# Performance work log

Measured on AMD Instinct MI355X. Metric: run time of the kernel, lower is better.

Reference implementation:

```python
import jax, jax.numpy as jnp
import numpy as np

B, S, D, H = 1, 4096, 1024, 16
HD = D // H  # 64


def setup_inputs() -> dict:
    key = jax.random.key(0)
    k1, k2, k3, k4, k5 = jax.random.split(key, 5)
    hidden_states = jax.random.normal(k1, (B, S, D), dtype=jnp.float32)
    # rotary frequencies: freqs_cis[s, j] = exp(i * s * theta^(-2j/HD)), stored as (cos, sin)
    inv_freq = 1.0 / (10000.0 ** (jnp.arange(0, HD, 2, dtype=jnp.float32) / HD))  # [HD/2]
    angles = jnp.arange(S, dtype=jnp.float32)[:, None] * inv_freq[None, :]        # [S, HD/2]
    freqs_cis = jnp.stack([jnp.cos(angles), jnp.sin(angles)], axis=-1)            # [S, HD/2, 2]
    attention_mask = jnp.ones((B, S), dtype=jnp.float32)
    scale = 1.0 / np.sqrt(D)
    wq = jax.random.normal(k2, (D, D), dtype=jnp.float32) * scale
    wk = jax.random.normal(k3, (D, D), dtype=jnp.float32) * scale
    wv = jax.random.normal(k4, (D, D), dtype=jnp.float32) * scale
    wo = jax.random.normal(k5, (D, D), dtype=jnp.float32) * scale
    return {"hidden_states": hidden_states, "freqs_cis": freqs_cis,
            "attention_mask": attention_mask, "wq": wq, "wk": wk, "wv": wv, "wo": wo}


def _apply_rope(x, freqs_cis):
    # x: [B, S, H, HD]; freqs_cis: [S, HD/2, 2] (cos, sin)
    b, s, h, hd = x.shape
    xr = x.reshape(b, s, h, hd // 2, 2)
    a, bb = xr[..., 0], xr[..., 1]
    cos = freqs_cis[None, :s, None, :, 0]
    sin = freqs_cis[None, :s, None, :, 1]
    out_r = a * cos - bb * sin
    out_i = a * sin + bb * cos
    return jnp.stack([out_r, out_i], axis=-1).reshape(b, s, h, hd)


def reference(hidden_states, freqs_cis, attention_mask, wq, wk, wv, wo):
    b, s, d = hidden_states.shape
    scaling = HD ** -0.5
    q = (hidden_states @ wq).reshape(b, s, H, HD)
    k = (hidden_states @ wk).reshape(b, s, H, HD)
    v = (hidden_states @ wv).reshape(b, s, H, HD)
    q = _apply_rope(q, freqs_cis)
    k = _apply_rope(k, freqs_cis)
    # [B, H, S, S] scores, exactly as the torch module materializes them
    scores = jnp.einsum('bqhd,bkhd->bhqk', q, k) * scaling
    mask_add = (1.0 - attention_mask)[:, None, None, :] * -10000.0  # [B,1,1,S]
    scores = scores + mask_add
    attn = jax.nn.softmax(scores.astype(jnp.float32), axis=-1).astype(q.dtype)
    out = jnp.einsum('bhqk,bkhd->bqhd', attn, v).reshape(b, s, d)
    return out @ wo
```

## Files before the change

### kernel.cpp

```cpp
#include <hip/hip_runtime.h>
#include <stdint.h>

#define S_LEN 4096
#define DMODEL 1024
#define NH 16
#define HDIM 64
#define KSPLIT 2
#define KCHUNK (S_LEN / KSPLIT)
#define LOG2E 1.44269504088896340736f

typedef __attribute__((ext_vector_type(8))) __bf16 bf16x8;
typedef __attribute__((ext_vector_type(4))) __bf16 bf16x4;
typedef __attribute__((ext_vector_type(2))) __bf16 bf16x2;
typedef __attribute__((ext_vector_type(4))) float f32x4;
typedef __attribute__((ext_vector_type(16))) float f32x16;
typedef __attribute__((ext_vector_type(4))) unsigned int uint32x4;

__global__ __launch_bounds__(256) void convert_f32_bf16(const float* __restrict__ src,
                                                        __bf16* __restrict__ dst,
                                                        const float* __restrict__ mask,
                                                        float* __restrict__ maskadd) {
  int idx = blockIdx.x * 256 + threadIdx.x;
  f32x4 v = ((const f32x4*)src)[idx];
  bf16x4 o;
#pragma unroll
  for (int i = 0; i < 4; ++i) o[i] = (__bf16)v[i];
  ((bf16x4*)dst)[idx] = o;
  if (idx < S_LEN) maskadd[idx] = (1.0f - mask[idx]) * (-10000.0f * LOG2E);
}

template <typename T>
__global__ __launch_bounds__(256) void transpose_tiles(const T* __restrict__ src,
                                                       __bf16* __restrict__ dst,
                                                       int R, int C) {
  src += (size_t)blockIdx.z * R * C;
  dst += (size_t)blockIdx.z * R * C;
  __shared__ __bf16 tile[64][65];
  const int r0 = blockIdx.y * 64, c0 = blockIdx.x * 64;
  const int t = threadIdx.x;
  const int col = t & 63, rsub = t >> 6;
#pragma unroll
  for (int i = 0; i < 16; ++i) {
    int r = rsub + i * 4;
    tile[r][col] = (__bf16)src[(size_t)(r0 + r) * C + (c0 + col)];
  }
  __syncthreads();
#pragma unroll
  for (int i = 0; i < 16; ++i) {
    int r = rsub + i * 4;
    dst[(size_t)(c0 + r) * R + (r0 + col)] = tile[col][r];
  }
}

template <int EPI>
__global__ __launch_bounds__(256) void gemm_bt(const __bf16* __restrict__ A,
                                               const __bf16* __restrict__ BT,
                                               __bf16* __restrict__ Cq,
                                               __bf16* __restrict__ Ck,
                                               __bf16* __restrict__ Cv,
                                               float* __restrict__ Cout,
                                               int Kdim, int Ndim) {
  __shared__ __align__(16) __bf16 At[128][40];
  __shared__ __align__(16) __bf16 Bt[128][40];
  const int t = threadIdx.x;
  const int wave = t >> 6, lane = t & 63;
  const int wr = wave >> 1, wc = wave & 1;
  const int lrow = lane & 15, lk = lane >> 4;
  const int bm = blockIdx.x, bn = blockIdx.y;

  f32x4 acc[4][4];
#pragma unroll
  for (int i = 0; i < 4; ++i)
#pragma unroll
    for (int j = 0; j < 4; ++j) acc[i][j] = f32x4{0.f, 0.f, 0.f, 0.f};

  const int arow0 = bm * 128, brow0 = bn * 128;
  for (int k0 = 0; k0 < Kdim; k0 += 32) {
    __syncthreads();
#pragma unroll
    for (int u = 0; u < 2; ++u) {
      int idx = t + u * 256;
      int row = idx >> 2, col = (idx & 3) * 8;
      *(bf16x8*)&At[row][col] =
          *(const bf16x8*)&A[(size_t)(arow0 + row) * Kdim + (k0 + col)];
      *(bf16x8*)&Bt[row][col] =
          *(const bf16x8*)&BT[(size_t)(brow0 + row) * Kdim + (k0 + col)];
    }
    __syncthreads();
    bf16x8 af[4], bfr[4];
#pragma unroll
    for (int mi = 0; mi < 4; ++mi)
      af[mi] = *(const bf16x8*)&At[wr * 64 + mi * 16 + lrow][lk * 8];
#pragma unroll
    for (int ni = 0; ni < 4; ++ni)
      bfr[ni] = *(const bf16x8*)&Bt[wc * 64 + ni * 16 + lrow][lk * 8];
#pragma unroll
    for (int mi = 0; mi < 4; ++mi)
#pragma unroll
      for (int ni = 0; ni < 4; ++ni)
        acc[mi][ni] =
            __builtin_amdgcn_mfma_f32_16x16x32_bf16(af[mi], bfr[ni], acc[mi][ni], 0, 0, 0);
  }

  const int rb = bm * 128 + wr * 64 + lk * 4;
  const int cb = bn * 128 + wc * 64 + lrow;
#pragma unroll
  for (int mi = 0; mi < 4; ++mi)
#pragma unroll
    for (int ni = 0; ni < 4; ++ni) {
      int c = cb + ni * 16;
#pragma unroll
      for (int r = 0; r < 4; ++r) {
        int row = rb + mi * 16 + r;
        float v = acc[mi][ni][r];
        if (EPI == 0) {
          Cout[(size_t)row * Ndim + c] = v;
        } else {
          int type = c >> 10, d = c & 1023;
          int hh = d >> 6, hd = d & 63;
          __bf16* dp = (type == 0) ? Cq : (type == 1) ? Ck : Cv;
          dp[((size_t)hh * S_LEN + row) * HDIM + hd] = (__bf16)v;
        }
      }
    }
}

__global__ __launch_bounds__(256) void rope_kernel(__bf16* __restrict__ Q,
                                                   __bf16* __restrict__ Kb,
                                                   const float* __restrict__ freqs) {
  size_t idx = (size_t)blockIdx.x * 256 + threadIdx.x;
  int i = idx & 31;
  size_t rest = idx >> 5;
  int s = rest & 4095;
  int h = (int)(rest >> 12);
  float c = freqs[(s * 32 + i) * 2 + 0];
  float sn = freqs[(s * 32 + i) * 2 + 1];
  size_t base = ((size_t)h * S_LEN + s) * HDIM + 2 * i;
  float qa = (float)Q[base], qb = (float)Q[base + 1];
  Q[base] = (__bf16)(qa * c - qb * sn);
  Q[base + 1] = (__bf16)(qa * sn + qb * c);
  float ka = (float)Kb[base], kb2 = (float)Kb[base + 1];
  Kb[base] = (__bf16)(ka * c - kb2 * sn);
  Kb[base + 1] = (__bf16)(ka * sn + kb2 * c);
}

__global__ __launch_bounds__(256, 4) void attn_split(const __bf16* __restrict__ Q,
                                                     const __bf16* __restrict__ Kmat,
                                                     const __bf16* __restrict__ Vt,
                                                     const float* __restrict__ maskadd,
                                                     float* __restrict__ Opart,
                                                     float* __restrict__ Lpart) {
  __shared__ __align__(16) __bf16 Kl[2][64][64];
  __shared__ __align__(16) __bf16 Vl[2][64][64];

  const int t = threadIdx.x;
  const int id = blockIdx.x;
  const int swz = (id & 7) * 128 + (id >> 3);
  const int h = swz >> 6;
  const int rem = swz & 63;
  const int qb = rem >> 1;
  const int split = rem & 1;
  const int k0 = split * KCHUNK;
  const int wave = t >> 6, lane = t & 63;
  const int lq = lane & 31, hi = lane >> 5;
  const int sw = lq & 7;

  const __bf16* Kh = Kmat + (size_t)h * S_LEN * HDIM;
  const __bf16* Vh = Vt + (size_t)h * HDIM * S_LEN;

  const int sr = t >> 2;
  const int sc0 = (t & 3) * 2;
  const int scs0 = (sc0 ^ (sr & 7)) * 8;
  const int scs1 = ((sc0 + 1) ^ (sr & 7)) * 8;
  const __bf16* Kgb = Kh + (size_t)sr * HDIM + sc0 * 8;
  const __bf16* Vgb = Vh + (size_t)sr * S_LEN + sc0 * 8;

  uint32x4 kreg0, kreg1, vreg0, vreg1;
  kreg0 = *(const uint32x4*)(Kgb + (size_t)k0 * HDIM);
  kreg1 = *(const uint32x4*)(Kgb + (size_t)k0 * HDIM + 8);
  vreg0 = *(const uint32x4*)(Vgb + k0);
  vreg1 = *(const uint32x4*)(Vgb + k0 + 8);
  *(uint32x4*)&Kl[0][sr][scs0] = kreg0;
  *(uint32x4*)&Kl[0][sr][scs1] = kreg1;
  *(uint32x4*)&Vl[0][sr][scs0] = vreg0;
  *(uint32x4*)&Vl[0][sr][scs1] = vreg1;

  const __bf16* Qh = Q + ((size_t)h * S_LEN + qb * 128 + wave * 32 + lq) * HDIM;
  bf16x8 qf[4];
#pragma unroll
  for (int ds = 0; ds < 4; ++ds) qf[ds] = *(const bf16x8*)(Qh + ds * 16 + hi * 8);

  __syncthreads();

  const float SCL = 0.125f * LOG2E;
  float l = 0.f;
  f32x16 o0, o1;
#pragma unroll
  for (int r = 0; r < 16; ++r) { o0[r] = 0.f; o1[r] = 0.f; }

  for (int it = 0; it < KCHUNK / 64; ++it) {
    const int cur = it & 1;
    const int kb = k0 + it * 64;

    if (it < KCHUNK / 64 - 1) {
      kreg0 = *(const uint32x4*)(Kgb + (size_t)(kb + 64) * HDIM);
      kreg1 = *(const uint32x4*)(Kgb + (size_t)(kb + 64) * HDIM + 8);
      vreg0 = *(const uint32x4*)(Vgb + (kb + 64));
      vreg1 = *(const uint32x4*)(Vgb + (kb + 64) + 8);
    }

    f32x16 p0, p1;
#pragma unroll
    for (int r = 0; r < 16; ++r) { p0[r] = 0.f; p1[r] = 0.f; }
    __builtin_amdgcn_s_setprio(1);
#pragma unroll
    for (int ds = 0; ds < 4; ++ds) {
      int sg = ((ds << 1) | hi) ^ sw;
      bf16x8 kf0 = *(const bf16x8*)&Kl[cur][lq][sg * 8];
      p0 = __builtin_amdgcn_mfma_f32_32x32x16_bf16(kf0, qf[ds], p0, 0, 0, 0);
    }
#pragma unroll
    for (int ds = 0; ds < 4; ++ds) {
      int sg = ((ds << 1) | hi) ^ sw;
      bf16x8 kf1 = *(const bf16x8*)&Kl[cur][lq + 32][sg * 8];
      p1 = __builtin_amdgcn_mfma_f32_32x32x16_bf16(kf1, qf[ds], p1, 0, 0, 0);
    }
    __builtin_amdgcn_s_setprio(0);

#pragma unroll
    for (int tq = 0; tq < 4; ++tq) {
      f32x4 ma0 = *(const f32x4*)&maskadd[kb + tq * 8 + hi * 4];
      f32x4 ma1 = *(const f32x4*)&maskadd[kb + 32 + tq * 8 + hi * 4];
#pragma unroll
      for (int c = 0; c < 4; ++c) {
        p0[tq * 4 + c] = exp2f(fmaf(p0[tq * 4 + c], SCL, ma0[c]));
        p1[tq * 4 + c] = exp2f(fmaf(p1[tq * 4 + c], SCL, ma1[c]));
      }
    }
    {
      float a0 = (p0[0] + p0[1]) + (p0[2] + p0[3]);
      float a1 = (p0[4] + p0[5]) + (p0[6] + p0[7]);
      float a2 = (p0[8] + p0[9]) + (p0[10] + p0[11]);
      float a3 = (p0[12] + p0[13]) + (p0[14] + p0[15]);
      float b0 = (p1[0] + p1[1]) + (p1[2] + p1[3]);
      float b1 = (p1[4] + p1[5]) + (p1[6] + p1[7]);
      float b2 = (p1[8] + p1[9]) + (p1[10] + p1[11]);
      float b3 = (p1[12] + p1[13]) + (p1[14] + p1[15]);
      float ps = ((a0 + a1) + (a2 + a3)) + ((b0 + b1) + (b2 + b3));
      ps += __shfl_xor(ps, 32);
      l += ps;
    }

    unsigned int tt0[8], tt1[8];
#pragma unroll
    for (int tp = 0; tp < 8; ++tp) {
      bf16x2 w0, w1;
      w0[0] = (__bf16)p0[2 * tp]; w0[1] = (__bf16)p0[2 * tp + 1];
      w1[0] = (__bf16)p1[2 * tp]; w1[1] = (__bf16)p1[2 * tp + 1];
      tt0[tp] = __builtin_bit_cast(unsigned int, w0);
      tt1[tp] = __builtin_bit_cast(unsigned int, w1);
    }

#pragma unroll
    for (int ks = 0; ks < 4; ++ks) {
      unsigned int b0, b1, b2, b3;
      if (ks == 0)      { b0 = tt0[0]; b1 = tt0[1]; b2 = tt0[2]; b3 = tt0[3]; }
      else if (ks == 1) { b0 = tt0[4]; b1 = tt0[5]; b2 = tt0[6]; b3 = tt0[7]; }
      else if (ks == 2) { b0 = tt1[0]; b1 = tt1[1]; b2 = tt1[2]; b3 = tt1[3]; }
      else              { b0 = tt1[4]; b1 = tt1[5]; b2 = tt1[6]; b3 = tt1[7]; }
      unsigned int send0 = hi ? b0 : b2;
      unsigned int send1 = hi ? b1 : b3;
      unsigned int r0 = (unsigned int)__shfl_xor((int)send0, 32);
      unsigned int r1 = (unsigned int)__shfl_xor((int)send1, 32);
      uint32x4 pb;
      pb[0] = hi ? r0 : b0;
      pb[1] = hi ? r1 : b1;
      pb[2] = hi ? b2 : r0;
      pb[3] = hi ? b3 : r1;
      bf16x8 pbv = __builtin_bit_cast(bf16x8, pb);
      int sg = ((ks << 1) | hi) ^ sw;
      bf16x8 v0 = *(const bf16x8*)&Vl[cur][lq][sg * 8];
      bf16x8 v1 = *(const bf16x8*)&Vl[cur][lq + 32][sg * 8];
      __builtin_amdgcn_s_setprio(1);
      o0 = __builtin_amdgcn_mfma_f32_32x32x16_bf16(v0, pbv, o0, 0, 0, 0);
      o1 = __builtin_amdgcn_mfma_f32_32x32x16_bf16(v1, pbv, o1, 0, 0, 0);
      __builtin_amdgcn_s_setprio(0);
    }

    if (it < KCHUNK / 64 - 1) {
      *(uint32x4*)&Kl[cur ^ 1][sr][scs0] = kreg0;
      *(uint32x4*)&Kl[cur ^ 1][sr][scs1] = kreg1;
      *(uint32x4*)&Vl[cur ^ 1][sr][scs0] = vreg0;
      *(uint32x4*)&Vl[cur ^ 1][sr][scs1] = vreg1;
      __syncthreads();
    }
  }

  const int qrow = qb * 128 + wave * 32 + lq;
  float* Op = Opart + (((size_t)split * NH + h) * S_LEN + qrow) * 64;
#pragma unroll
  for (int tq = 0; tq < 4; ++tq) {
    f32x4 a, b;
#pragma unroll
    for (int c = 0; c < 4; ++c) { a[c] = o0[tq * 4 + c]; b[c] = o1[tq * 4 + c]; }
    *(f32x4*)(Op + tq * 8 + hi * 4) = a;
    *(f32x4*)(Op + 32 + tq * 8 + hi * 4) = b;
  }
  if (hi == 0) Lpart[((size_t)split * NH + h) * S_LEN + qrow] = l;
}

__global__ __launch_bounds__(256) void attn_merge(const float* __restrict__ Opart,
                                                  const float* __restrict__ Lpart,
                                                  __bf16* __restrict__ AO) {
  int idx = blockIdx.x * 256 + threadIdx.x;
  int dd = (idx & 15) * 4;
  int hq = idx >> 4;
  int q = hq & (S_LEN - 1), h = hq >> 12;
  float lA = Lpart[hq], lB = Lpart[NH * S_LEN + hq];
  float inv = 1.0f / fmaxf(lA + lB, 1e-30f);
  f32x4 a = *(const f32x4*)&Opart[(size_t)hq * 64 + dd];
  f32x4 b = *(const f32x4*)&Opart[((size_t)NH * S_LEN + hq) * 64 + dd];
  bf16x4 o;
#pragma unroll
  for (int c = 0; c < 4; ++c) o[c] = (__bf16)((a[c] + b[c]) * inv);
  *(bf16x4*)&AO[(size_t)q * DMODEL + h * HDIM + dd] = o;
}

extern "C" void kernel_launch(void* const* d_in, const int* in_sizes, int n_in,
                              void* d_out, int out_size, void* d_ws, size_t ws_size,
                              hipStream_t stream) {
  const float* X = (const float*)d_in[0];
  const float* freqs = (const float*)d_in[1];
  const float* mask = (const float*)d_in[2];
  const float* wq = (const float*)d_in[3];
  const float* wk = (const float*)d_in[4];
  const float* wv = (const float*)d_in[5];
  const float* wo = (const float*)d_in[6];
  float* out = (float*)d_out;

  __bf16* WTqkv = (__bf16*)d_ws;
  __bf16* WoT = WTqkv + 3072 * 1024;
  __bf16* Xb = WoT + 1024 * 1024;
  __bf16* Qb = Xb + (size_t)S_LEN * DMODEL;
  __bf16* Kb = Qb + (size_t)NH * S_LEN * HDIM;
  __bf16* Vb = Kb + (size_t)NH * S_LEN * HDIM;
  __bf16* Vtb = Vb + (size_t)NH * S_LEN * HDIM;
  __bf16* AO = Vb;

  float* Opart = (float*)(Vtb + (size_t)NH * S_LEN * HDIM);
  float* Lpart = Opart + (size_t)KSPLIT * NH * S_LEN * 64;
  float* maskadd = Lpart + (size_t)KSPLIT * NH * S_LEN;

  convert_f32_bf16<<<dim3(S_LEN * DMODEL / 1024), 256, 0, stream>>>(X, Xb, mask, maskadd);

  transpose_tiles<float><<<dim3(16, 16, 1), 256, 0, stream>>>(wq, WTqkv, 1024, 1024);
  transpose_tiles<float><<<dim3(16, 16, 1), 256, 0, stream>>>(wk, WTqkv + 1024 * 1024, 1024, 1024);
  transpose_tiles<float><<<dim3(16, 16, 1), 256, 0, stream>>>(wv, WTqkv + 2 * 1024 * 1024, 1024, 1024);
  transpose_tiles<float><<<dim3(16, 16, 1), 256, 0, stream>>>(wo, WoT, 1024, 1024);

  gemm_bt<1><<<dim3(32, 24), 256, 0, stream>>>(Xb, WTqkv, Qb, Kb, Vb, nullptr, 1024, 3072);

  rope_kernel<<<dim3((NH * S_LEN * 32) / 256), 256, 0, stream>>>(Qb, Kb, freqs);

  transpose_tiles<__bf16><<<dim3(1, 64, NH), 256, 0, stream>>>(Vb, Vtb, S_LEN, HDIM);

  attn_split<<<dim3(32 * NH * KSPLIT), 256, 0, stream>>>(Qb, Kb, Vtb, maskadd, Opart, Lpart);
  attn_merge<<<dim3(NH * S_LEN * 16 / 256), 256, 0, stream>>>(Opart, Lpart, AO);

  gemm_bt<0><<<dim3(32, 8), 256, 0, stream>>>(AO, WoT, nullptr, nullptr, nullptr, out, 1024, 1024);
}
```

Before: 235.6 us.

## Process two 32-row query tiles per wave in split attention kernel

Each wave now handles 64 query rows (two 32-row sub-tiles) instead of 32, so each block covers 256 queries and the grid is halved to 512 blocks. K and V fragments loaded from LDS are reused across both query sub-tiles, which halves LDS reads and global K/V traffic per query. In exchange, register pressure roughly doubles for the accumulators (launch bounds relaxed from 4 to 2 blocks per SM), and the smaller grid of 512 blocks may underfill the 256 CUs.

```diff
diff --git a/kernel.cpp b/kernel.cpp
--- a/kernel.cpp
+++ b/kernel.cpp
@@ -144,7 +144,7 @@
   Kb[base + 1] = (__bf16)(ka * sn + kb2 * c);
 }
 
-__global__ __launch_bounds__(256, 4) void attn_split(const __bf16* __restrict__ Q,
+__global__ __launch_bounds__(256, 2) void attn_split(const __bf16* __restrict__ Q,
                                                      const __bf16* __restrict__ Kmat,
                                                      const __bf16* __restrict__ Vt,
                                                      const float* __restrict__ maskadd,
@@ -155,9 +155,9 @@
 
   const int t = threadIdx.x;
   const int id = blockIdx.x;
-  const int swz = (id & 7) * 128 + (id >> 3);
-  const int h = swz >> 6;
-  const int rem = swz & 63;
+  const int swz = (id & 7) * 64 + (id >> 3);
+  const int h = swz >> 5;
+  const int rem = swz & 31;
   const int qb = rem >> 1;
   const int split = rem & 1;
   const int k0 = split * KCHUNK;
@@ -185,18 +185,21 @@
   *(uint32x4*)&Vl[0][sr][scs0] = vreg0;
   *(uint32x4*)&Vl[0][sr][scs1] = vreg1;
 
-  const __bf16* Qh = Q + ((size_t)h * S_LEN + qb * 128 + wave * 32 + lq) * HDIM;
-  bf16x8 qf[4];
-#pragma unroll
-  for (int ds = 0; ds < 4; ++ds) qf[ds] = *(const bf16x8*)(Qh + ds * 16 + hi * 8);
+  const __bf16* Qh = Q + ((size_t)h * S_LEN + qb * 256 + wave * 64 + lq) * HDIM;
+  bf16x8 qfA[4], qfB[4];
+#pragma unroll
+  for (int ds = 0; ds < 4; ++ds) {
+    qfA[ds] = *(const bf16x8*)(Qh + ds * 16 + hi * 8);
+    qfB[ds] = *(const bf16x8*)(Qh + (size_t)32 * HDIM + ds * 16 + hi * 8);
+  }
 
   __syncthreads();
 
   const float SCL = 0.125f * LOG2E;
-  float l = 0.f;
-  f32x16 o0, o1;
-#pragma unroll
-  for (int r = 0; r < 16; ++r) { o0[r] = 0.f; o1[r] = 0.f; }
+  float lA = 0.f, lB = 0.f;
+  f32x16 oA0, oA1, oB0, oB1;
+#pragma unroll
+  for (int r = 0; r < 16; ++r) { oA0[r] = 0.f; oA1[r] = 0.f; oB0[r] = 0.f; oB1[r] = 0.f; }
 
   for (int it = 0; it < KCHUNK / 64; ++it) {
     const int cur = it & 1;
@@ -209,21 +212,23 @@
       vreg1 = *(const uint32x4*)(Vgb + (kb + 64) + 8);
     }
 
-    f32x16 p0, p1;
-#pragma unroll
-    for (int r = 0; r < 16; ++r) { p0[r] = 0.f; p1[r] = 0.f; }
+    f32x16 pA0, pA1, pB0, pB1;
+#pragma unroll
+    for (int r = 0; r < 16; ++r) { pA0[r] = 0.f; pA1[r] = 0.f; pB0[r] = 0.f; pB1[r] = 0.f; }
     __builtin_amdgcn_s_setprio(1);
 #pragma unroll
     for (int ds = 0; ds < 4; ++ds) {
       int sg = ((ds << 1) | hi) ^ sw;
       bf16x8 kf0 = *(const bf16x8*)&Kl[cur][lq][sg * 8];
-      p0 = __builtin_amdgcn_mfma_f32_32x32x16_bf16(kf0, qf[ds], p0, 0, 0, 0);
+      pA0 = __builtin_amdgcn_mfma_f32_32x32x16_bf16(kf0, qfA[ds], pA0, 0, 0, 0);
+      pB0 = __builtin_amdgcn_mfma_f32_32x32x16_bf16(kf0, qfB[ds], pB0, 0, 0, 0);
     }
 #pragma unroll
     for (int ds = 0; ds < 4; ++ds) {
       int sg = ((ds << 1) | hi) ^ sw;
       bf16x8 kf1 = *(const bf16x8*)&Kl[cur][lq + 32][sg * 8];
-      p1 = __builtin_amdgcn_mfma_f32_32x32x16_bf16(kf1, qf[ds], p1, 0, 0, 0);
+      pA1 = __builtin_amdgcn_mfma_f32_32x32x16_bf16(kf1, qfA[ds], pA1, 0, 0, 0);
+      pB1 = __builtin_amdgcn_mfma_f32_32x32x16_bf16(kf1, qfB[ds], pB1, 0, 0, 0);
     }
     __builtin_amdgcn_s_setprio(0);
 
@@ -233,57 +238,85 @@
       f32x4 ma1 = *(const f32x4*)&maskadd[kb + 32 + tq * 8 + hi * 4];
 #pragma unroll
       for (int c = 0; c < 4; ++c) {
-        p0[tq * 4 + c] = exp2f(fmaf(p0[tq * 4 + c], SCL, ma0[c]));
-        p1[tq * 4 + c] = exp2f(fmaf(p1[tq * 4 + c], SCL, ma1[c]));
+        pA0[tq * 4 + c] = exp2f(fmaf(pA0[tq * 4 + c], SCL, ma0[c]));
+        pB0[tq * 4 + c] = exp2f(fmaf(pB0[tq * 4 + c], SCL, ma0[c]));
+        pA1[tq * 4 + c] = exp2f(fmaf(pA1[tq * 4 + c], SCL, ma1[c]));
+        pB1[tq * 4 + c] = exp2f(fmaf(pB1[tq * 4 + c], SCL, ma1[c]));
       }
     }
     {
-      float a0 = (p0[0] + p0[1]) + (p0[2] + p0[3]);
-      float a1 = (p0[4] + p0[5]) + (p0[6] + p0[7]);
-      float a2 = (p0[8] + p0[9]) + (p0[10] + p0[11]);
-      float a3 = (p0[12] + p0[13]) + (p0[14] + p0[15]);
-      float b0 = (p1[0] + p1[1]) + (p1[2] + p1[3]);
-      float b1 = (p1[4] + p1[5]) + (p1[6] + p1[7]);
-      float b2 = (p1[8] + p1[9]) + (p1[10] + p1[11]);
-      float b3 = (p1[12] + p1[13]) + (p1[14] + p1[15]);
+      float a0 = (pA0[0] + pA0[1]) + (pA0[2] + pA0[3]);
+      float a1 = (pA0[4] + pA0[5]) + (pA0[6] + pA0[7]);
+      float a2 = (pA0[8] + pA0[9]) + (pA0[10] + pA0[11]);
+      float a3 = (pA0[12] + pA0[13]) + (pA0[14] + pA0[15]);
+      float b0 = (pA1[0] + pA1[1]) + (pA1[2] + pA1[3]);
+      float b1 = (pA1[4] + pA1[5]) + (pA1[6] + pA1[7]);
+      float b2 = (pA1[8] + pA1[9]) + (pA1[10] + pA1[11]);
+      float b3 = (pA1[12] + pA1[13]) + (pA1[14] + pA1[15]);
       float ps = ((a0 + a1) + (a2 + a3)) + ((b0 + b1) + (b2 + b3));
       ps += __shfl_xor(ps, 32);
-      l += ps;
-    }
-
-    unsigned int tt0[8], tt1[8];
+      lA += ps;
+    }
+    {
+      float a0 = (pB0[0] + pB0[1]) + (pB0[2] + pB0[3]);
+      float a1 = (pB0[4] + pB0[5]) + (pB0[6] + pB0[7]);
+      float a2 = (pB0[8] + pB0[9]) + (pB0[10] + pB0[11]);
+      float a3 = (pB0[12] + pB0[13]) + (pB0[14] + pB0[15]);
+      float b0 = (pB1[0] + pB1[1]) + (pB1[2] + pB1[3]);
+      float b1 = (pB1[4] + pB1[5]) + (pB1[6] + pB1[7]);
+      float b2 = (pB1[8] + pB1[9]) + (pB1[10] + pB1[11]);
+      float b3 = (pB1[12] + pB1[13]) + (pB1[14] + pB1[15]);
+      float ps = ((a0 + a1) + (a2 + a3)) + ((b0 + b1) + (b2 + b3));
+      ps += __shfl_xor(ps, 32);
+      lB += ps;
+    }
+
+    unsigned int tA0[8], tA1[8], tB0[8], tB1[8];
 #pragma unroll
     for (int tp = 0; tp < 8; ++tp) {
-      bf16x2 w0, w1;
-      w0[0] = (__bf16)p0[2 * tp]; w0[1] = (__bf16)p0[2 * tp + 1];
-      w1[0] = (__bf16)p1[2 * tp]; w1[1] = (__bf16)p1[2 * tp + 1];
-      tt0[tp] = __builtin_bit_cast(unsigned int, w0);
-      tt1[tp] = __builtin_bit_cast(unsigned int, w1);
+      bf16x2 wa0, wa1, wb0, wb1;
+      wa0[0] = (__bf16)pA0[2 * tp]; wa0[1] = (__bf16)pA0[2 * tp + 1];
+      wa1[0] = (__bf16)pA1[2 * tp]; wa1[1] = (__bf16)pA1[2 * tp + 1];
+      wb0[0] = (__bf16)pB0[2 * tp]; wb0[1] = (__bf16)pB0[2 * tp + 1];
+      wb1[0] = (__bf16)pB1[2 * tp]; wb1[1] = (__bf16)pB1[2 * tp + 1];
+      tA0[tp] = __builtin_bit_cast(unsigned int, wa0);
+      tA1[tp] = __builtin_bit_cast(unsigned int, wa1);
+      tB0[tp] = __builtin_bit_cast(unsigned int, wb0);
+      tB1[tp] = __builtin_bit_cast(unsigned int, wb1);
     }
 
 #pragma unroll
     for (int ks = 0; ks < 4; ++ks) {
-      unsigned int b0, b1, b2, b3;
-      if (ks == 0)      { b0 = tt0[0]; b1 = tt0[1]; b2 = tt0[2]; b3 = tt0[3]; }
-      else if (ks == 1) { b0 = tt0[4]; b1 = tt0[5]; b2 = tt0[6]; b3 = tt0[7]; }
-      else if (ks == 2) { b0 = tt1[0]; b1 = tt1[1]; b2 = tt1[2]; b3 = tt1[3]; }
-      else              { b0 = tt1[4]; b1 = tt1[5]; b2 = tt1[6]; b3 = tt1[7]; }
-      unsigned int send0 = hi ? b0 : b2;
-      unsigned int send1 = hi ? b1 : b3;
-      unsigned int r0 = (unsigned int)__shfl_xor((int)send0, 32);
-      unsigned int r1 = (unsigned int)__shfl_xor((int)send1, 32);
-      uint32x4 pb;
-      pb[0] = hi ? r0 : b0;
-      pb[1] = hi ? r1 : b1;
-      pb[2] = hi ? b2 : r0;
-      pb[3] = hi ? b3 : r1;
-      bf16x8 pbv = __builtin_bit_cast(bf16x8, pb);
+      unsigned int a0, a1, a2, a3, b0, b1, b2, b3;
+      if (ks == 0)      { a0 = tA0[0]; a1 = tA0[1]; a2 = tA0[2]; a3 = tA0[3];
+                          b0 = tB0[0]; b1 = tB0[1]; b2 = tB0[2]; b3 = tB0[3]; }
+      else if (ks == 1) { a0 = tA0[4]; a1 = tA0[5]; a2 = tA0[6]; a3 = tA0[7];
+                          b0 = tB0[4]; b1 = tB0[5]; b2 = tB0[6]; b3 = tB0[7]; }
+      else if (ks == 2) { a0 = tA1[0]; a1 = tA1[1]; a2 = tA1[2]; a3 = tA1[3];
+                          b0 = tB1[0]; b1 = tB1[1]; b2 = tB1[2]; b3 = tB1[3]; }
+      else              { a0 = tA1[4]; a1 = tA1[5]; a2 = tA1[6]; a3 = tA1[7];
+                          b0 = tB1[4]; b1 = tB1[5]; b2 = tB1[6]; b3 = tB1[7]; }
+      unsigned int sa0 = hi ? a0 : a2, sa1 = hi ? a1 : a3;
+      unsigned int sb0 = hi ? b0 : b2, sb1 = hi ? b1 : b3;
+      unsigned int ra0 = (unsigned int)__shfl_xor((int)sa0, 32);
+      unsigned int ra1 = (unsigned int)__shfl_xor((int)sa1, 32);
+      unsigned int rb0 = (unsigned int)__shfl_xor((int)sb0, 32);
+      unsigned int rb1 = (unsigned int)__shfl_xor((int)sb1, 32);
+      uint32x4 fa, fb;
+      fa[0] = hi ? ra0 : a0; fa[1] = hi ? ra1 : a1;
+      fa[2] = hi ? a2 : ra0; fa[3] = hi ? a3 : ra1;
+      fb[0] = hi ? rb0 : b0; fb[1] = hi ? rb1 : b1;
+      fb[2] = hi ? b2 : rb0; fb[3] = hi ? b3 : rb1;
+      bf16x8 fav = __builtin_bit_cast(bf16x8, fa);
+      bf16x8 fbv = __builtin_bit_cast(bf16x8, fb);
       int sg = ((ks << 1) | hi) ^ sw;
       bf16x8 v0 = *(const bf16x8*)&Vl[cur][lq][sg * 8];
       bf16x8 v1 = *(const bf16x8*)&Vl[cur][lq + 32][sg * 8];
       __builtin_amdgcn_s_setprio(1);
-      o0 = __builtin_amdgcn_mfma_f32_32x32x16_bf16(v0, pbv, o0, 0, 0, 0);
-      o1 = __builtin_amdgcn_mfma_f32_32x32x16_bf16(v1, pbv, o1, 0, 0, 0);
+      oA0 = __builtin_amdgcn_mfma_f32_32x32x16_bf16(v0, fav, oA0, 0, 0, 0);
+      oA1 = __builtin_amdgcn_mfma_f32_32x32x16_bf16(v1, fav, oA1, 0, 0, 0);
+      oB0 = __builtin_amdgcn_mfma_f32_32x32x16_bf16(v0, fbv, oB0, 0, 0, 0);
+      oB1 = __builtin_amdgcn_mfma_f32_32x32x16_bf16(v1, fbv, oB1, 0, 0, 0);
       __builtin_amdgcn_s_setprio(0);
     }
 
@@ -296,17 +329,26 @@
     }
   }
 
-  const int qrow = qb * 128 + wave * 32 + lq;
-  float* Op = Opart + (((size_t)split * NH + h) * S_LEN + qrow) * 64;
+  const int qrowA = qb * 256 + wave * 64 + lq;
+  float* OpA = Opart + (((size_t)split * NH + h) * S_LEN + qrowA) * 64;
+  float* OpB = OpA + (size_t)32 * 64;
 #pragma unroll
   for (int tq = 0; tq < 4; ++tq) {
-    f32x4 a, b;
-#pragma unroll
-    for (int c = 0; c < 4; ++c) { a[c] = o0[tq * 4 + c]; b[c] = o1[tq * 4 + c]; }
-    *(f32x4*)(Op + tq * 8 + hi * 4) = a;
-    *(f32x4*)(Op + 32 + tq * 8 + hi * 4) = b;
-  }
-  if (hi == 0) Lpart[((size_t)split * NH + h) * S_LEN + qrow] = l;
+    f32x4 a, b, c, d;
+#pragma unroll
+    for (int cc = 0; cc < 4; ++cc) {
+      a[cc] = oA0[tq * 4 + cc]; b[cc] = oA1[tq * 4 + cc];
+      c[cc] = oB0[tq * 4 + cc]; d[cc] = oB1[tq * 4 + cc];
+    }
+    *(f32x4*)(OpA + tq * 8 + hi * 4) = a;
+    *(f32x4*)(OpA + 32 + tq * 8 + hi * 4) = b;
+    *(f32x4*)(OpB + tq * 8 + hi * 4) = c;
+    *(f32x4*)(OpB + 32 + tq * 8 + hi * 4) = d;
+  }
+  if (hi == 0) {
+    Lpart[((size_t)split * NH + h) * S_LEN + qrowA] = lA;
+    Lpart[((size_t)split * NH + h) * S_LEN + qrowA + 32] = lB;
+  }
 }
 
 __global__ __launch_bounds__(256) void attn_merge(const float* __restrict__ Opart,
@@ -364,7 +406,7 @@
 
   transpose_tiles<__bf16><<<dim3(1, 64, NH), 256, 0, stream>>>(Vb, Vtb, S_LEN, HDIM);
 
-  attn_split<<<dim3(32 * NH * KSPLIT), 256, 0, stream>>>(Qb, Kb, Vtb, maskadd, Opart, Lpart);
+  attn_split<<<dim3(16 * NH * KSPLIT), 256, 0, stream>>>(Qb, Kb, Vtb, maskadd, Opart, Lpart);
   attn_merge<<<dim3(NH * S_LEN * 16 / 256), 256, 0, stream>>>(Opart, Lpart, AO);
 
   gemm_bt<0><<<dim3(32, 8), 256, 0, stream>>>(AO, WoT, nullptr, nullptr, nullptr, out, 1024, 1024);
```

Measured after the change: 216.9 us. -8.0%, faster.
